# Performance work log

Measured on AMD Instinct MI355X. Metric: run time of the kernel, lower is better.

Reference implementation:

```python
import jax, jax.numpy as jnp
import numpy as np

B, C_LEN, Q_LEN, H = 16, 2048, 128, 128
NEG = -1000000000.0


def setup_inputs() -> dict:
    key = jax.random.key(0)
    k1, k2, k3, k4, k5 = jax.random.split(key, 5)
    context = jax.random.normal(k1, (B, C_LEN, H), dtype=jnp.float32)
    query = jax.random.normal(k2, (B, Q_LEN, H), dtype=jnp.float32)
    W = jax.random.normal(k3, (3 * H,), dtype=jnp.float32) * (1.0 / np.sqrt(3 * H))
    context_mask = jax.random.randint(k4, (B, C_LEN), 0, 2).astype(jnp.int32)
    query_mask = jax.random.randint(k5, (B, Q_LEN), 0, 2).astype(jnp.int32)
    return {"context": context, "query": query, "W": W,
            "context_mask": context_mask, "query_mask": query_mask}


def reference(context, query, W, context_mask, query_mask):
    h = context.shape[-1]
    # Decompose W([c; q; c*q]) into three rank-1 terms -> avoid (B,c,q,3h) tensor.
    w_c, w_q, w_cq = W[:h], W[h:2 * h], W[2 * h:]
    s_c = context @ w_c                                   # (B, c_len)
    s_q = query @ w_q                                     # (B, q_len)
    s_cq = jnp.einsum('bch,bqh->bcq', context * w_cq, query)
    S = s_c[:, :, None] + s_q[:, None, :] + s_cq          # (B, c_len, q_len)
    # query mask -> C2Q attention
    S = jnp.where(query_mask[:, None, :] == 0, NEG, S)
    a = jax.nn.softmax(S, axis=-1)
    c2q = jnp.einsum('bcq,bqh->bch', a, query)
    # context mask -> Q2C attention over max-over-query scores
    S_for_q2c = jnp.where(context_mask[:, :, None] == 0, NEG, S)
    max_q = jnp.max(S_for_q2c, axis=-1)                   # (B, c_len)
    max_q = jnp.where(context_mask == 0, NEG, max_q)
    b = jax.nn.softmax(max_q, axis=-1)
    q2c = jnp.einsum('bc,bch->bh', b, context)            # (B, h)
    G = jnp.concatenate(
        [context, c2q, context * c2q, context * q2c[:, None, :]], axis=-1)
    return G  # (B, c_len, 4h)
```

## Files before the change

kernel.cpp:

```cpp
#include <hip/hip_runtime.h>
#include <math.h>

#define B_ 16
#define C_ 2048
#define Q_ 128
#define H_ 128
#define NEGV (-1000000000.0f)
#define REC_ 136

typedef short short8 __attribute__((ext_vector_type(8)));
typedef float f32x16 __attribute__((ext_vector_type(16)));
typedef float f32x4 __attribute__((ext_vector_type(4)));

__device__ __forceinline__ short f2bf(float f) {
  unsigned u = __builtin_bit_cast(unsigned, f);
  u += 0x7fffu + ((u >> 16) & 1u);
  return (short)(u >> 16);
}

__device__ __forceinline__ int swz(int row, int ch) {
  return row * 128 + (((ch ^ (row & 7)) & 15) << 3);
}

__device__ __forceinline__ void nt_store4(float* p, float4 v) {
  __builtin_nontemporal_store(__builtin_bit_cast(f32x4, v), (f32x4*)p);
}
__device__ __forceinline__ void nt_store1(float* p, float v) {
  __builtin_nontemporal_store(v, p);
}

__device__ __forceinline__ float wave_max(float v) {
#pragma unroll
  for (int off = 32; off; off >>= 1) v = fmaxf(v, __shfl_xor(v, off, 64));
  return v;
}
__device__ __forceinline__ float wave_sum(float v) {
#pragma unroll
  for (int off = 32; off; off >>= 1) v += __shfl_xor(v, off, 64);
  return v;
}

__global__ __launch_bounds__(256) void k0_pre(const float* __restrict__ qry,
                                              const float* __restrict__ W,
                                              const int* __restrict__ qmask,
                                              short* __restrict__ qb,
                                              float* __restrict__ sqm_g) {
  int t = blockIdx.x * 256 + threadIdx.x;
  int row = t >> 5, l = t & 31;
  float4 v = *(const float4*)&qry[(size_t)row * H_ + 4 * l];
  float4 wq = *(const float4*)&W[H_ + 4 * l];
  float s = v.x * wq.x + v.y * wq.y + v.z * wq.z + v.w * wq.w;
  short4 pk;
  pk.x = f2bf(v.x); pk.y = f2bf(v.y); pk.z = f2bf(v.z); pk.w = f2bf(v.w);
  *(short4*)&qb[(size_t)row * H_ + 4 * l] = pk;
  s += __shfl_xor(s, 1, 64);
  s += __shfl_xor(s, 2, 64);
  s += __shfl_xor(s, 4, 64);
  s += __shfl_xor(s, 8, 64);
  s += __shfl_xor(s, 16, 64);
  if (l == 0) sqm_g[row] = qmask[row] ? s : -1e12f;
}

__global__ __launch_bounds__(512, 4) void k1_main(
    const float* __restrict__ ctx, const short* __restrict__ qb,
    const float* __restrict__ W, const int* __restrict__ cmask,
    const float* __restrict__ sqm_g, float* __restrict__ out,
    float* __restrict__ pw) {
  __shared__ short QTs[16384];
  __shared__ short Xs[8192];
  __shared__ float scv[64];
  __shared__ float sqm[128];
  __shared__ float pm_lds[4][64];
  __shared__ float ps_lds[4][64];
  __shared__ float mcv[64];
  __shared__ float wcv[64];
  __shared__ float mzl[2];
  __shared__ float pq2[2][128];

  int b = blockIdx.x >> 5;
  int ct = blockIdx.x & 31;
  int tid = threadIdx.x;
  int bc0 = b * C_ + ct * 64;

  {
    int c = tid >> 3, part = tid & 7;
    const float* crow = ctx + (size_t)(bc0 + c) * H_;
    float* orow = out + (size_t)(bc0 + c) * (4 * H_);
    float wsum = 0.f;
#pragma unroll
    for (int jj = 0; jj < 4; jj++) {
      int k = part + 8 * jj;
      float4 v = *(const float4*)&crow[4 * k];
      nt_store4(&orow[4 * k], v);
      float4 wc = *(const float4*)&W[4 * k];
      float4 wq = *(const float4*)&W[2 * H_ + 4 * k];
      wsum += v.x * wc.x + v.y * wc.y + v.z * wc.z + v.w * wc.w;
      short4 xp;
      xp.x = f2bf(v.x * wq.x);
      xp.y = f2bf(v.y * wq.y);
      xp.z = f2bf(v.z * wq.z);
      xp.w = f2bf(v.w * wq.w);
      *(short4*)&Xs[swz(c, k >> 1) + (k & 1) * 4] = xp;
    }
    wsum += __shfl_xor(wsum, 1, 64);
    wsum += __shfl_xor(wsum, 2, 64);
    wsum += __shfl_xor(wsum, 4, 64);
    if (part == 0) scv[c] = wsum;
  }
  {
    int qp = tid >> 3, p = tid & 7;
    const short* r0 = qb + ((size_t)b * Q_ + 2 * qp) * H_;
    const short* r1 = r0 + H_;
#pragma unroll
    for (int pass = 0; pass < 2; pass++) {
      int h0 = p * 8 + pass * 64;
      short8 v0 = *(const short8*)&r0[h0];
      short8 v1 = *(const short8*)&r1[h0];
#pragma unroll
      for (int e = 0; e < 8; e++) {
        short2 pr;
        pr.x = v0[e];
        pr.y = v1[e];
        *(short2*)&QTs[swz(h0 + e, qp >> 2) + ((2 * qp) & 7)] = pr;
      }
    }
  }
  if (tid < 128) sqm[tid] = sqm_g[b * Q_ + tid];
  __syncthreads();

  int w = tid >> 6, lane = tid & 63;
  int lq = lane & 31, kg = lane >> 5;

  int wm = w >> 1, wn = w & 1;
  f32x16 acc;
#pragma unroll
  for (int r = 0; r < 16; r++) acc[r] = 0.f;
  {
    const short* arow = qb + ((size_t)b * Q_ + wm * 32 + lq) * H_;
    int rB = wn * 32 + lq;
#pragma unroll
    for (int ks = 0; ks < 8; ks++) {
      int ch = 2 * ks + kg;
      short8 a = *(const short8*)&arow[ch * 8];
      short8 bb = *(const short8*)&Xs[swz(rB, ch)];
      acc = __builtin_amdgcn_mfma_f32_32x32x16_bf16(a, bb, acc, 0, 0, 0);
    }
  }

  int cL = wn * 32 + lq;
  float scc = scv[cL];
  float pmax = -3e38f;
#pragma unroll
  for (int g = 0; g < 4; g++) {
    int q0 = wm * 32 + 8 * g + 4 * kg;
    float4 s4 = *(const float4*)&sqm[q0];
    float sv[4] = {s4.x, s4.y, s4.z, s4.w};
#pragma unroll
    for (int r = 0; r < 4; r++) {
      float Sv = acc[4 * g + r] + scc + sv[r];
      acc[4 * g + r] = Sv;
      pmax = fmaxf(pmax, Sv);
    }
  }
  pmax = fmaxf(pmax, __shfl_xor(pmax, 32, 64));
  if (lane < 32) pm_lds[wm][cL] = pmax;
  __syncthreads();

  float M = fmaxf(fmaxf(pm_lds[0][cL], pm_lds[1][cL]),
                  fmaxf(pm_lds[2][cL], pm_lds[3][cL]));
  if (wm == 0 && lane < 32) {
    mcv[cL] = cmask[bc0 + cL] ? M : NEGV;
  }
  float psum = 0.f;
#pragma unroll
  for (int g = 0; g < 4; g++) {
    int q0 = wm * 32 + 8 * g + 4 * kg;
    float e0 = __expf(acc[4 * g + 0] - M);
    float e1 = __expf(acc[4 * g + 1] - M);
    float e2 = __expf(acc[4 * g + 2] - M);
    float e3 = __expf(acc[4 * g + 3] - M);
    psum += e0 + e1 + e2 + e3;
    short4 pk;
    pk.x = f2bf(e0); pk.y = f2bf(e1); pk.z = f2bf(e2); pk.w = f2bf(e3);
    *(short4*)&Xs[swz(cL, q0 >> 3) + (q0 & 7)] = pk;
  }
  psum += __shfl_xor(psum, 32, 64);
  if (lane < 32) ps_lds[wm][cL] = psum;
  __syncthreads();

  if (tid < 64) {
    float mv = mcv[tid];
    float lm = wave_max(mv);
    float ew = __expf(mv - lm);
    wcv[tid] = ew;
    float lz = wave_sum(ew);
    if (tid == 0) { mzl[0] = lm; mzl[1] = lz; }
  }

  int wm2 = w & 1, wn2 = w >> 1;
  f32x16 o;
#pragma unroll
  for (int r = 0; r < 16; r++) o[r] = 0.f;
  {
    int rA = wm2 * 32 + lq, rB = wn2 * 32 + lq;
#pragma unroll
    for (int ks = 0; ks < 8; ks++) {
      int ch = 2 * ks + kg;
      short8 af = *(const short8*)&Xs[swz(rA, ch)];
      short8 bf_ = *(const short8*)&QTs[swz(rB, ch)];
      o = __builtin_amdgcn_mfma_f32_32x32x16_bf16(af, bf_, o, 0, 0, 0);
    }
  }
  __syncthreads();

  int h = wn2 * 32 + lq;
  float part = 0.f;
#pragma unroll
  for (int g = 0; g < 4; g++) {
    int c0 = wm2 * 32 + 8 * g + 4 * kg;
    float4 z0 = *(const float4*)&ps_lds[0][c0];
    float4 z1 = *(const float4*)&ps_lds[1][c0];
    float4 z2 = *(const float4*)&ps_lds[2][c0];
    float4 z3 = *(const float4*)&ps_lds[3][c0];
    float zz[4] = {z0.x + z1.x + z2.x + z3.x, z0.y + z1.y + z2.y + z3.y,
                   z0.z + z1.z + z2.z + z3.z, z0.w + z1.w + z2.w + z3.w};
#pragma unroll
    for (int r = 0; r < 4; r++) {
      int c = c0 + r;
      float rz = 1.f / zz[r];
      size_t ro = (size_t)(bc0 + c) * (4 * H_);
      float ov = o[4 * g + r] * rz;
      float cv = ctx[(size_t)(bc0 + c) * H_ + h];
      nt_store1(&out[ro + H_ + h], ov);
      nt_store1(&out[ro + 2 * H_ + h], ov * cv);
      part += wcv[c] * cv;
    }
  }
  part += __shfl_xor(part, 32, 64);
  if (kg == 0) pq2[wm2][h] = part;
  __syncthreads();

  float* rec = pw + (size_t)blockIdx.x * REC_;
  if (tid < 128) rec[8 + tid] = pq2[0][tid] + pq2[1][tid];
  if (tid == 128) rec[0] = mzl[0];
  if (tid == 129) rec[1] = mzl[1];
}

__global__ __launch_bounds__(256) void k4_out(const float* __restrict__ ctx,
                                              const float* __restrict__ pw,
                                              float* __restrict__ out) {
  __shared__ float q2cs[128];
  int b = blockIdx.x >> 5;
  int ct = blockIdx.x & 31;
  int tid = threadIdx.x;
  int bc0 = b * C_ + ct * 64;

  if (tid < 128) {
    const float* base = pw + (size_t)b * 32 * REC_;
    float Mg = -3e38f;
#pragma unroll
    for (int t = 0; t < 32; t++) Mg = fmaxf(Mg, base[t * REC_]);
    float Zg = 0.f, s = 0.f;
#pragma unroll
    for (int t = 0; t < 32; t++) {
      float et = __expf(base[t * REC_] - Mg);
      Zg += et * base[t * REC_ + 1];
      s += et * base[t * REC_ + 8 + tid];
    }
    q2cs[tid] = s / Zg;
  }
  __syncthreads();

  int c = tid >> 2, part = tid & 3;
  const float* crow = ctx + (size_t)(bc0 + c) * H_;
  float* orow = out + (size_t)(bc0 + c) * (4 * H_) + 3 * H_;
#pragma unroll
  for (int jj = 0; jj < 8; jj++) {
    int k = part + 4 * jj;
    float4 v = *(const float4*)&crow[4 * k];
    float4 g = *(const float4*)&q2cs[4 * k];
    nt_store4(&orow[4 * k],
              make_float4(v.x * g.x, v.y * g.y, v.z * g.z, v.w * g.w));
  }
}

extern "C" void kernel_launch(void* const* d_in, const int* in_sizes, int n_in,
                              void* d_out, int out_size, void* d_ws,
                              size_t ws_size, hipStream_t stream) {
  const float* ctx = (const float*)d_in[0];
  const float* qry = (const float*)d_in[1];
  const float* W = (const float*)d_in[2];
  const int* cmask = (const int*)d_in[3];
  const int* qmask = (const int*)d_in[4];
  float* out = (float*)d_out;

  short* qb = (short*)d_ws;
  float* sqm_g = (float*)((char*)d_ws + (size_t)B_ * Q_ * H_ * sizeof(short));
  float* pw = sqm_g + B_ * Q_;

  k0_pre<<<256, 256, 0, stream>>>(qry, W, qmask, qb, sqm_g);
  k1_main<<<B_ * 32, 512, 0, stream>>>(ctx, qb, W, cmask, sqm_g, out, pw);
  k4_out<<<B_ * 32, 256, 0, stream>>>(ctx, pw, out);
}
```

Baseline: 30.44 us.

## Halve context tile per block and precompute transposed bf16 query in prepass

The main kernel now processes 32 context rows per 256-thread block, which doubles the grid. The prepass writes a transposed bf16 copy of the query plus partial query-weight dot products, so the main kernel reads the second GEMM's B operand straight from global memory and no longer builds a transposed query tile in LDS. This cuts LDS use and per-block setup, aiming for more resident blocks and better latency hiding. The output stores for c2q are now ordinary stores instead of nontemporal, and the final kernel reduces 64 partial records per batch instead of 32.

Result: slower. 38.88 us (+27.7%).

```diff
diff --git a/kernel.cpp b/kernel.cpp
--- a/kernel.cpp
+++ b/kernel.cpp
@@ -25,9 +25,6 @@
 __device__ __forceinline__ void nt_store4(float* p, float4 v) {
   __builtin_nontemporal_store(__builtin_bit_cast(f32x4, v), (f32x4*)p);
 }
-__device__ __forceinline__ void nt_store1(float* p, float v) {
-  __builtin_nontemporal_store(v, p);
-}
 
 __device__ __forceinline__ float wave_max(float v) {
 #pragma unroll
@@ -42,45 +39,60 @@
 
 __global__ __launch_bounds__(256) void k0_pre(const float* __restrict__ qry,
                                               const float* __restrict__ W,
-                                              const int* __restrict__ qmask,
                                               short* __restrict__ qb,
-                                              float* __restrict__ sqm_g) {
-  int t = blockIdx.x * 256 + threadIdx.x;
-  int row = t >> 5, l = t & 31;
-  float4 v = *(const float4*)&qry[(size_t)row * H_ + 4 * l];
-  float4 wq = *(const float4*)&W[H_ + 4 * l];
-  float s = v.x * wq.x + v.y * wq.y + v.z * wq.z + v.w * wq.w;
-  short4 pk;
-  pk.x = f2bf(v.x); pk.y = f2bf(v.y); pk.z = f2bf(v.z); pk.w = f2bf(v.w);
-  *(short4*)&qb[(size_t)row * H_ + 4 * l] = pk;
+                                              short* __restrict__ qbT,
+                                              float* __restrict__ sq4) {
+  __shared__ short T[32][64];
+  int bid = blockIdx.x;
+  int b = bid >> 3, hs = (bid >> 1) & 3, qh = bid & 1;
+  int tid = threadIdx.x;
+  int r = tid >> 2, p = tid & 3;
+  int q = qh * 64 + r;
+  const float* qrow = qry + ((size_t)b * Q_ + q) * H_ + hs * 32;
+  float s = 0.f;
+#pragma unroll
+  for (int j = 0; j < 2; j++) {
+    int k = p + 4 * j;
+    float4 v = *(const float4*)&qrow[4 * k];
+    float4 wq = *(const float4*)&W[H_ + hs * 32 + 4 * k];
+    s += v.x * wq.x + v.y * wq.y + v.z * wq.z + v.w * wq.w;
+    short4 pk;
+    pk.x = f2bf(v.x); pk.y = f2bf(v.y); pk.z = f2bf(v.z); pk.w = f2bf(v.w);
+    *(short4*)&qb[((size_t)b * Q_ + q) * H_ + hs * 32 + 4 * k] = pk;
+    T[4 * k + 0][r] = pk.x;
+    T[4 * k + 1][r] = pk.y;
+    T[4 * k + 2][r] = pk.z;
+    T[4 * k + 3][r] = pk.w;
+  }
   s += __shfl_xor(s, 1, 64);
   s += __shfl_xor(s, 2, 64);
-  s += __shfl_xor(s, 4, 64);
-  s += __shfl_xor(s, 8, 64);
-  s += __shfl_xor(s, 16, 64);
-  if (l == 0) sqm_g[row] = qmask[row] ? s : -1e12f;
-}
-
-__global__ __launch_bounds__(512, 4) void k1_main(
+  if (p == 0) sq4[(hs * B_ + b) * Q_ + q] = s;
+  __syncthreads();
+  int hl = tid >> 3, pp = tid & 7;
+  short8 v = *(const short8*)&T[hl][pp * 8];
+  *(short8*)&qbT[((size_t)b * H_ + hs * 32 + hl) * Q_ + qh * 64 + pp * 8] = v;
+}
+
+__global__ __launch_bounds__(256, 4) void k1_main(
     const float* __restrict__ ctx, const short* __restrict__ qb,
-    const float* __restrict__ W, const int* __restrict__ cmask,
-    const float* __restrict__ sqm_g, float* __restrict__ out,
+    const short* __restrict__ qbT, const float* __restrict__ W,
+    const int* __restrict__ cmask, const int* __restrict__ qmask,
+    const float* __restrict__ sq4, float* __restrict__ out,
     float* __restrict__ pw) {
-  __shared__ short QTs[16384];
-  __shared__ short Xs[8192];
-  __shared__ float scv[64];
+  __shared__ short Xs[32 * 128];
+  __shared__ float scv[32];
   __shared__ float sqm[128];
-  __shared__ float pm_lds[4][64];
-  __shared__ float ps_lds[4][64];
-  __shared__ float mcv[64];
-  __shared__ float wcv[64];
+  __shared__ float pm_lds[4][32];
+  __shared__ float ps_lds[4][32];
+  __shared__ float mcv[32];
+  __shared__ float wcv[32];
   __shared__ float mzl[2];
-  __shared__ float pq2[2][128];
-
-  int b = blockIdx.x >> 5;
-  int ct = blockIdx.x & 31;
+  __shared__ float pq2[128];
+
+  int b = blockIdx.x >> 6;
+  int ct = blockIdx.x & 63;
   int tid = threadIdx.x;
-  int bc0 = b * C_ + ct * 64;
+  int bc0 = b * C_ + ct * 32;
 
   {
     int c = tid >> 3, part = tid & 7;
@@ -107,52 +119,36 @@
     wsum += __shfl_xor(wsum, 4, 64);
     if (part == 0) scv[c] = wsum;
   }
-  {
-    int qp = tid >> 3, p = tid & 7;
-    const short* r0 = qb + ((size_t)b * Q_ + 2 * qp) * H_;
-    const short* r1 = r0 + H_;
-#pragma unroll
-    for (int pass = 0; pass < 2; pass++) {
-      int h0 = p * 8 + pass * 64;
-      short8 v0 = *(const short8*)&r0[h0];
-      short8 v1 = *(const short8*)&r1[h0];
-#pragma unroll
-      for (int e = 0; e < 8; e++) {
-        short2 pr;
-        pr.x = v0[e];
-        pr.y = v1[e];
-        *(short2*)&QTs[swz(h0 + e, qp >> 2) + ((2 * qp) & 7)] = pr;
-      }
-    }
-  }
-  if (tid < 128) sqm[tid] = sqm_g[b * Q_ + tid];
+  if (tid < 128) {
+    float s = sq4[(0 * B_ + b) * Q_ + tid] + sq4[(1 * B_ + b) * Q_ + tid] +
+              sq4[(2 * B_ + b) * Q_ + tid] + sq4[(3 * B_ + b) * Q_ + tid];
+    sqm[tid] = qmask[b * Q_ + tid] ? s : -1e12f;
+  }
   __syncthreads();
 
   int w = tid >> 6, lane = tid & 63;
   int lq = lane & 31, kg = lane >> 5;
 
-  int wm = w >> 1, wn = w & 1;
   f32x16 acc;
 #pragma unroll
   for (int r = 0; r < 16; r++) acc[r] = 0.f;
   {
-    const short* arow = qb + ((size_t)b * Q_ + wm * 32 + lq) * H_;
-    int rB = wn * 32 + lq;
+    const short* arow = qb + ((size_t)b * Q_ + w * 32 + lq) * H_;
 #pragma unroll
     for (int ks = 0; ks < 8; ks++) {
       int ch = 2 * ks + kg;
       short8 a = *(const short8*)&arow[ch * 8];
-      short8 bb = *(const short8*)&Xs[swz(rB, ch)];
+      short8 bb = *(const short8*)&Xs[swz(lq, ch)];
       acc = __builtin_amdgcn_mfma_f32_32x32x16_bf16(a, bb, acc, 0, 0, 0);
     }
   }
 
-  int cL = wn * 32 + lq;
+  int cL = lq;
   float scc = scv[cL];
   float pmax = -3e38f;
 #pragma unroll
   for (int g = 0; g < 4; g++) {
-    int q0 = wm * 32 + 8 * g + 4 * kg;
+    int q0 = w * 32 + 8 * g + 4 * kg;
     float4 s4 = *(const float4*)&sqm[q0];
     float sv[4] = {s4.x, s4.y, s4.z, s4.w};
 #pragma unroll
@@ -163,18 +159,18 @@
     }
   }
   pmax = fmaxf(pmax, __shfl_xor(pmax, 32, 64));
-  if (lane < 32) pm_lds[wm][cL] = pmax;
+  if (lane < 32) pm_lds[w][cL] = pmax;
   __syncthreads();
 
   float M = fmaxf(fmaxf(pm_lds[0][cL], pm_lds[1][cL]),
                   fmaxf(pm_lds[2][cL], pm_lds[3][cL]));
-  if (wm == 0 && lane < 32) {
+  if (w == 0 && lane < 32) {
     mcv[cL] = cmask[bc0 + cL] ? M : NEGV;
   }
   float psum = 0.f;
 #pragma unroll
   for (int g = 0; g < 4; g++) {
-    int q0 = wm * 32 + 8 * g + 4 * kg;
+    int q0 = w * 32 + 8 * g + 4 * kg;
     float e0 = __expf(acc[4 * g + 0] - M);
     float e1 = __expf(acc[4 * g + 1] - M);
     float e2 = __expf(acc[4 * g + 2] - M);
@@ -185,39 +181,38 @@
     *(short4*)&Xs[swz(cL, q0 >> 3) + (q0 & 7)] = pk;
   }
   psum += __shfl_xor(psum, 32, 64);
-  if (lane < 32) ps_lds[wm][cL] = psum;
+  if (lane < 32) ps_lds[w][cL] = psum;
   __syncthreads();
 
   if (tid < 64) {
-    float mv = mcv[tid];
+    float mv = mcv[tid & 31];
     float lm = wave_max(mv);
     float ew = __expf(mv - lm);
-    wcv[tid] = ew;
-    float lz = wave_sum(ew);
+    float lz = 0.5f * wave_sum(ew);
+    if (tid < 32) wcv[tid] = ew;
     if (tid == 0) { mzl[0] = lm; mzl[1] = lz; }
   }
 
-  int wm2 = w & 1, wn2 = w >> 1;
   f32x16 o;
 #pragma unroll
   for (int r = 0; r < 16; r++) o[r] = 0.f;
   {
-    int rA = wm2 * 32 + lq, rB = wn2 * 32 + lq;
+    const short* brow = qbT + ((size_t)b * H_ + w * 32 + lq) * Q_;
 #pragma unroll
     for (int ks = 0; ks < 8; ks++) {
       int ch = 2 * ks + kg;
-      short8 af = *(const short8*)&Xs[swz(rA, ch)];
-      short8 bf_ = *(const short8*)&QTs[swz(rB, ch)];
-      o = __builtin_amdgcn_mfma_f32_32x32x16_bf16(af, bf_, o, 0, 0, 0);
-    }
-  }
-  __syncthreads();
-
-  int h = wn2 * 32 + lq;
+      short8 af = *(const short8*)&Xs[swz(lq, ch)];
+      short8 bb = *(const short8*)&brow[ch * 8];
+      o = __builtin_amdgcn_mfma_f32_32x32x16_bf16(af, bb, o, 0, 0, 0);
+    }
+  }
+  __syncthreads();
+
+  int h = w * 32 + lq;
   float part = 0.f;
 #pragma unroll
   for (int g = 0; g < 4; g++) {
-    int c0 = wm2 * 32 + 8 * g + 4 * kg;
+    int c0 = 8 * g + 4 * kg;
     float4 z0 = *(const float4*)&ps_lds[0][c0];
     float4 z1 = *(const float4*)&ps_lds[1][c0];
     float4 z2 = *(const float4*)&ps_lds[2][c0];
@@ -231,17 +226,17 @@
       size_t ro = (size_t)(bc0 + c) * (4 * H_);
       float ov = o[4 * g + r] * rz;
       float cv = ctx[(size_t)(bc0 + c) * H_ + h];
-      nt_store1(&out[ro + H_ + h], ov);
-      nt_store1(&out[ro + 2 * H_ + h], ov * cv);
+      out[ro + H_ + h] = ov;
+      out[ro + 2 * H_ + h] = ov * cv;
       part += wcv[c] * cv;
     }
   }
   part += __shfl_xor(part, 32, 64);
-  if (kg == 0) pq2[wm2][h] = part;
+  if (kg == 0) pq2[h] = part;
   __syncthreads();
 
   float* rec = pw + (size_t)blockIdx.x * REC_;
-  if (tid < 128) rec[8 + tid] = pq2[0][tid] + pq2[1][tid];
+  if (tid < 128) rec[8 + tid] = pq2[tid];
   if (tid == 128) rec[0] = mzl[0];
   if (tid == 129) rec[1] = mzl[1];
 }
@@ -256,13 +251,13 @@
   int bc0 = b * C_ + ct * 64;
 
   if (tid < 128) {
-    const float* base = pw + (size_t)b * 32 * REC_;
+    const float* base = pw + (size_t)b * 64 * REC_;
     float Mg = -3e38f;
 #pragma unroll
-    for (int t = 0; t < 32; t++) Mg = fmaxf(Mg, base[t * REC_]);
+    for (int t = 0; t < 64; t++) Mg = fmaxf(Mg, base[t * REC_]);
     float Zg = 0.f, s = 0.f;
-#pragma unroll
-    for (int t = 0; t < 32; t++) {
+#pragma unroll 8
+    for (int t = 0; t < 64; t++) {
       float et = __expf(base[t * REC_] - Mg);
       Zg += et * base[t * REC_ + 1];
       s += et * base[t * REC_ + 8 + tid];
@@ -295,10 +290,11 @@
   float* out = (float*)d_out;
 
   short* qb = (short*)d_ws;
-  float* sqm_g = (float*)((char*)d_ws + (size_t)B_ * Q_ * H_ * sizeof(short));
-  float* pw = sqm_g + B_ * Q_;
-
-  k0_pre<<<256, 256, 0, stream>>>(qry, W, qmask, qb, sqm_g);
-  k1_main<<<B_ * 32, 512, 0, stream>>>(ctx, qb, W, cmask, sqm_g, out, pw);
+  short* qbT = qb + (size_t)B_ * Q_ * H_;
+  float* sq4 = (float*)(qbT + (size_t)B_ * Q_ * H_);
+  float* pw = sq4 + 4 * B_ * Q_;
+
+  k0_pre<<<128, 256, 0, stream>>>(qry, W, qb, qbT, sq4);
+  k1_main<<<B_ * 64, 256, 0, stream>>>(ctx, qb, qbT, W, cmask, qmask, sq4, out, pw);
   k4_out<<<B_ * 32, 256, 0, stream>>>(ctx, pw, out);
 }
```
